# Optimization experiments

Measured on AMD Instinct MI355X. Metric: run time of the kernel, lower is better.

The kernel has to match this reference:

```python
import jax, jax.numpy as jnp
import numpy as np

N_FFT = 512
HOP = N_FFT // 4  # torch.stft default hop_length
TWO_PI = 2.0 * np.pi


def _stft_phase(x):
    """torch.stft(x, n_fft=512, return_complex=True) phase: center reflect-pad,
    rectangular window, onesided rfft. Returns [F, T'] with F = n_fft//2+1."""
    pad = N_FFT // 2
    xp = jnp.pad(x, (pad, pad), mode='reflect')
    n_frames = (xp.shape[0] - N_FFT) // HOP + 1
    idx = (np.arange(n_frames, dtype=np.int32)[:, None] * HOP
           + np.arange(N_FFT, dtype=np.int32)[None, :])
    frames = xp[idx]                      # [T', n_fft]
    spec = jnp.fft.rfft(frames, axis=-1)  # [T', F]
    return jnp.angle(spec).T              # [F, T']


def _anti_wrap(x):
    return jnp.abs(x - jnp.round(x / TWO_PI) * TWO_PI)


def _gd(p):
    # banded matmul with gd_matrix == out[f] = p[f-1] - p[f], out[0] = -p[0]
    return jnp.concatenate([-p[:1], p[:-1] - p[1:]], axis=0)


def _iaf(p):
    # banded matmul with iaf_matrix along time axis
    return jnp.concatenate([-p[:, :1], p[:, :-1] - p[:, 1:]], axis=1)


def setup_inputs() -> dict:
    key = jax.random.key(0)
    k1, k2 = jax.random.split(key)
    T = 4194304  # 2^22 samples (~262 s @ 16 kHz)
    yd = jax.random.normal(k1, (T,), dtype=jnp.float32)
    td = jax.random.normal(k2, (T,), dtype=jnp.float32)
    return {"yd": yd, "td": td}


def reference(yd, td):
    pr = _stft_phase(yd)  # [F, T']
    pg = _stft_phase(td)
    ip_loss = jnp.mean(_anti_wrap(pr - pg))
    gd_loss = jnp.mean(_anti_wrap(_gd(pr) - _gd(pg)))
    iaf_loss = jnp.mean(_anti_wrap(_iaf(pr) - _iaf(pg)))
    return (ip_loss, gd_loss, iaf_loss)
```

## Files before the change

### kernel.cpp

```cpp
#include <hip/hip_runtime.h>
#include <math.h>

#define HOP     128
#define NSLOTS  256
#define FPW     8
#define PI_F    3.14159265358979323846f
#define PI2_F   1.57079632679489661923f
#define K8      0.70710678118654752440f

struct cpx { float x, y; };
__device__ __forceinline__ cpx cadd(cpx a, cpx b){ return {a.x+b.x, a.y+b.y}; }
__device__ __forceinline__ cpx csub(cpx a, cpx b){ return {a.x-b.x, a.y-b.y}; }
__device__ __forceinline__ cpx cmul(cpx a, cpx b){
    return {fmaf(a.x,b.x,-a.y*b.y), fmaf(a.x,b.y, a.y*b.x)};
}
__device__ __forceinline__ cpx cmulc(cpx a, cpx b){
    return {fmaf(a.x,b.x, a.y*b.y), fmaf(a.y,b.x,-a.x*b.y)};
}

__device__ __forceinline__ float abs_angle(float re, float im) {
    float a = fabsf(im), b = fabsf(re);
    float mn = fminf(a, b), mx = fmaxf(a, b);
    float t = __fdividef(mn, fmaxf(mx, 1e-37f));
    float t2 = t * t;
    float p = fmaf(t2, -0.0117212f, 0.05265332f);
    p = fmaf(t2, p, -0.11643287f);
    p = fmaf(t2, p, 0.19354346f);
    p = fmaf(t2, p, -0.33262347f);
    p = fmaf(t2, p, 0.99997726f);
    float r = t * p;
    r = (a > b) ? (PI2_F - r) : r;
    r = (re < 0.f) ? (PI_F - r) : r;
    return r;
}

__device__ __forceinline__ void dft8(cpx v[8]) {
    cpx a0=cadd(v[0],v[4]), a1=cadd(v[1],v[5]), a2=cadd(v[2],v[6]), a3=cadd(v[3],v[7]);
    cpx b0=csub(v[0],v[4]), b1=csub(v[1],v[5]), b2=csub(v[2],v[6]), b3=csub(v[3],v[7]);
    b1 = cpx{K8*(b1.x+b1.y), K8*(b1.y-b1.x)};
    b2 = cpx{b2.y, -b2.x};
    b3 = cpx{K8*(b3.y-b3.x), -K8*(b3.x+b3.y)};
    cpx c0=cadd(a0,a2), c2=csub(a0,a2);
    cpx c1=cadd(a1,a3), c3=csub(a1,a3); c3 = cpx{c3.y, -c3.x};
    cpx d0=cadd(b0,b2), d2=csub(b0,b2);
    cpx d1=cadd(b1,b3), d3=csub(b1,b3); d3 = cpx{d3.y, -d3.x};
    v[0]=cadd(c0,c1); v[4]=csub(c0,c1);
    v[2]=cadd(c2,c3); v[6]=csub(c2,c3);
    v[1]=cadd(d0,d1); v[5]=csub(d0,d1);
    v[3]=cadd(d2,d3); v[7]=csub(d2,d3);
}

__global__ __launch_bounds__(256) void phase_loss_kernel(
        const float* __restrict__ y, const float* __restrict__ g,
        float* __restrict__ acc, int* __restrict__ ticket,
        float* __restrict__ out, int T, int n_frames, float inv_count) {
    __shared__ float2 xch_all[4][576];
    __shared__ float wsum[3][4];
    __shared__ int is_last;

    const int tid  = threadIdx.x;
    const int lane = tid & 63;
    const int wid  = tid >> 6;
    float2* xch = xch_all[wid];

    cpx tw1[8], tw2[8];
    #pragma unroll
    for (int k = 0; k < 8; ++k) {
        float a1 = -(2.0f * PI_F / 512.0f) * (float)(lane * k);
        __sincosf(a1, &tw1[k].y, &tw1[k].x);
        float a2 = -(2.0f * PI_F / 64.0f) * (float)((lane & 7) * k);
        __sincosf(a2, &tw2[k].y, &tw2[k].x);
    }

    float ip = 0.f, gd = 0.f, iaf = 0.f;
    cpx Cp[5];
    const int chain = blockIdx.x * 4 + wid;
    const int t0 = chain * FPW;
    const bool havep = (t0 > 0);

    auto do_frame = [&](int t, bool accum, bool hp) {
        cpx v[8];
        const int base = t * HOP - 256 + lane;
        #pragma unroll
        for (int r = 0; r < 8; ++r) {
            int j = base + r * 64;
            j = (j < 0) ? -j : j;
            j = (j >= T) ? (2 * T - 2 - j) : j;
            v[r].x = y[j]; v[r].y = g[j];
        }
        dft8(v);
        #pragma unroll
        for (int k = 1; k < 8; ++k) v[k] = cmul(v[k], tw1[k]);
        #pragma unroll
        for (int k = 0; k < 8; ++k)
            xch[k * 72 + lane] = make_float2(v[k].x, v[k].y);
        __builtin_amdgcn_s_waitcnt(0xc07f);
        __builtin_amdgcn_wave_barrier();
        {
            const int ra = (lane >> 3) * 72 + (lane & 7);
            #pragma unroll
            for (int r = 0; r < 8; ++r) {
                float2 tmp = xch[ra + r * 8];
                v[r] = cpx{tmp.x, tmp.y};
            }
        }
        dft8(v);
        #pragma unroll
        for (int k = 1; k < 8; ++k) v[k] = cmul(v[k], tw2[k]);
        #pragma unroll
        for (int k = 0; k < 8; ++k)
            xch[k * 65 + lane] = make_float2(v[k].x, v[k].y);
        __builtin_amdgcn_s_waitcnt(0xc07f);
        __builtin_amdgcn_wave_barrier();
        {
            const int ra = (lane >> 3) * 65 + (lane & 7) * 8;
            #pragma unroll
            for (int r = 0; r < 8; ++r) {
                float2 tmp = xch[ra + r];
                v[r] = cpx{tmp.x, tmp.y};
            }
        }
        dft8(v);
        cpx Cc[5];
        const int src = (64 - lane) & 63;
        #pragma unroll
        for (int jj = 0; jj < 5; ++jj) {
            cpx zk = v[jj];
            cpx zn;
            zn.x = __shfl(v[7 - jj].x, src);
            zn.y = __shfl(v[7 - jj].y, src);
            if (lane == 0) zn = v[(8 - jj) & 7];
            float ur = zk.x + zn.x, ui = zk.y - zn.y;
            float vx = zk.x - zn.x, vy = zk.y + zn.y;
            Cc[jj].x = fmaf(ur, vy, -ui * vx);
            Cc[jj].y = fmaf(ur, vx,  ui * vy);
        }
        if (accum) {
            #pragma unroll
            for (int jj = 0; jj < 4; ++jj) {
                cpx cc = Cc[jj];
                float aw = abs_angle(cc.x, cc.y);
                ip += aw;
                cpx cm;
                cm.x = __shfl_up(cc.x, 1);
                cm.y = __shfl_up(cc.y, 1);
                if (jj > 0) {
                    cpx cw;
                    cw.x = __shfl(Cc[jj - 1].x, 63);
                    cw.y = __shfl(Cc[jj - 1].y, 63);
                    if (lane == 0) cm = cw;
                }
                cpx qg = cmulc(cm, cc);
                gd += (jj == 0 && lane == 0) ? aw : abs_angle(qg.x, qg.y);
                if (hp) {
                    cpx qi = cmulc(Cp[jj], cc);
                    iaf += abs_angle(qi.x, qi.y);
                } else {
                    iaf += aw;
                }
            }
            {
                cpx cc = Cc[4];
                cpx cm;
                cm.x = __shfl(Cc[3].x, 63);
                cm.y = __shfl(Cc[3].y, 63);
                if (lane == 0) {
                    float aw = abs_angle(cc.x, cc.y);
                    ip += aw;
                    cpx qg = cmulc(cm, cc);
                    gd += abs_angle(qg.x, qg.y);
                    if (hp) {
                        cpx qi = cmulc(Cp[4], cc);
                        iaf += abs_angle(qi.x, qi.y);
                    } else {
                        iaf += aw;
                    }
                }
            }
        }
        #pragma unroll
        for (int jj = 0; jj < 5; ++jj) Cp[jj] = Cc[jj];
    };

    if (t0 < n_frames) {
        #pragma unroll 1
        for (int c = -1; c < FPW; ++c) {
            int t = t0 + c;
            if (c == -1) { if (!havep) continue; }
            else if (t >= n_frames) break;
            do_frame(t, c >= 0, havep || c > 0);
        }
    }

    __syncthreads();
    for (int off = 32; off; off >>= 1) {
        ip  += __shfl_down(ip, off);
        gd  += __shfl_down(gd, off);
        iaf += __shfl_down(iaf, off);
    }
    if (lane == 0) { wsum[0][wid] = ip; wsum[1][wid] = gd; wsum[2][wid] = iaf; }
    __syncthreads();
    if (tid == 0) {
        const int slot = (int)(blockIdx.x & (NSLOTS - 1));
        atomicAdd(acc + 0 * NSLOTS + slot, wsum[0][0] + wsum[0][1] + wsum[0][2] + wsum[0][3]);
        atomicAdd(acc + 1 * NSLOTS + slot, wsum[1][0] + wsum[1][1] + wsum[1][2] + wsum[1][3]);
        atomicAdd(acc + 2 * NSLOTS + slot, wsum[2][0] + wsum[2][1] + wsum[2][2] + wsum[2][3]);
        __threadfence();
        is_last = (atomicAdd(ticket, 1) == (int)gridDim.x - 1);
    }
    __syncthreads();
    if (is_last) {
        for (int l = 0; l < 3; l++) {
            float vv = __hip_atomic_load(acc + l * NSLOTS + tid,
                                         __ATOMIC_RELAXED, __HIP_MEMORY_SCOPE_AGENT);
            for (int off = 32; off; off >>= 1) vv += __shfl_down(vv, off);
            if (lane == 0) wsum[l][wid] = vv;
        }
        __syncthreads();
        if (tid < 3)
            out[tid] = (wsum[tid][0] + wsum[tid][1] + wsum[tid][2] + wsum[tid][3]) * inv_count;
    }
}

extern "C" void kernel_launch(void* const* d_in, const int* in_sizes, int n_in,
                              void* d_out, int out_size, void* d_ws, size_t ws_size,
                              hipStream_t stream) {
    const float* y = (const float*)d_in[0];
    const float* g = (const float*)d_in[1];
    float* out = (float*)d_out;
    float* acc = (float*)d_ws;
    int* ticket = (int*)((char*)d_ws + 3 * NSLOTS * sizeof(float));
    const int T = in_sizes[0];
    const int n_frames = T / HOP + 1;
    const int n_chains = (n_frames + FPW - 1) / FPW;
    const int n_blocks = (n_chains + 3) / 4;

    hipMemsetAsync(d_ws, 0, 3 * NSLOTS * sizeof(float) + sizeof(int), stream);
    const float inv_count = 1.0f / (257.0f * (float)n_frames);
    phase_loss_kernel<<<n_blocks, 256, 0, stream>>>(y, g, acc, ticket, out,
                                                    T, n_frames, inv_count);
}
```

Before: 138.4 us.

## Use LDS exchanges instead of shuffles, fast-path interior loads, restructure frame loop

Result: no change. 136.1 us (-1.6%).

```diff
diff --git a/kernel.cpp b/kernel.cpp
--- a/kernel.cpp
+++ b/kernel.cpp
@@ -7,6 +7,9 @@
 #define PI_F    3.14159265358979323846f
 #define PI2_F   1.57079632679489661923f
 #define K8      0.70710678118654752440f
+
+#define LDS_FENCE() do { __asm__ volatile("" ::: "memory"); \
+                         __builtin_amdgcn_wave_barrier(); } while (0)
 
 struct cpx { float x, y; };
 __device__ __forceinline__ cpx cadd(cpx a, cpx b){ return {a.x+b.x, a.y+b.y}; }
@@ -50,11 +53,12 @@
     v[3]=cadd(d2,d3); v[7]=csub(d2,d3);
 }
 
-__global__ __launch_bounds__(256) void phase_loss_kernel(
+__global__ __launch_bounds__(256, 4) void phase_loss_kernel(
         const float* __restrict__ y, const float* __restrict__ g,
         float* __restrict__ acc, int* __restrict__ ticket,
         float* __restrict__ out, int T, int n_frames, float inv_count) {
     __shared__ float2 xch_all[4][576];
+    __shared__ float2 cl_all[4][258];
     __shared__ float wsum[3][4];
     __shared__ int is_last;
 
@@ -62,6 +66,7 @@
     const int lane = tid & 63;
     const int wid  = tid >> 6;
     float2* xch = xch_all[wid];
+    float2* Cl  = cl_all[wid] + 1;
 
     cpx tw1[8], tw2[8];
     #pragma unroll
@@ -74,28 +79,34 @@
 
     float ip = 0.f, gd = 0.f, iaf = 0.f;
     cpx Cp[5];
-    const int chain = blockIdx.x * 4 + wid;
-    const int t0 = chain * FPW;
-    const bool havep = (t0 > 0);
+    const int tmax_int = (T - 256) / HOP;
 
     auto do_frame = [&](int t, bool accum, bool hp) {
         cpx v[8];
         const int base = t * HOP - 256 + lane;
-        #pragma unroll
-        for (int r = 0; r < 8; ++r) {
-            int j = base + r * 64;
-            j = (j < 0) ? -j : j;
-            j = (j >= T) ? (2 * T - 2 - j) : j;
-            v[r].x = y[j]; v[r].y = g[j];
+        if (t >= 2 && t <= tmax_int) {
+            #pragma unroll
+            for (int r = 0; r < 8; ++r) {
+                int j = base + r * 64;
+                v[r].x = y[j]; v[r].y = g[j];
+            }
+        } else {
+            #pragma unroll
+            for (int r = 0; r < 8; ++r) {
+                int j = base + r * 64;
+                j = (j < 0) ? -j : j;
+                j = (j >= T) ? (2 * T - 2 - j) : j;
+                v[r].x = y[j]; v[r].y = g[j];
+            }
         }
         dft8(v);
         #pragma unroll
         for (int k = 1; k < 8; ++k) v[k] = cmul(v[k], tw1[k]);
+        LDS_FENCE();
         #pragma unroll
         for (int k = 0; k < 8; ++k)
             xch[k * 72 + lane] = make_float2(v[k].x, v[k].y);
-        __builtin_amdgcn_s_waitcnt(0xc07f);
-        __builtin_amdgcn_wave_barrier();
+        LDS_FENCE();
         {
             const int ra = (lane >> 3) * 72 + (lane & 7);
             #pragma unroll
@@ -107,11 +118,11 @@
         dft8(v);
         #pragma unroll
         for (int k = 1; k < 8; ++k) v[k] = cmul(v[k], tw2[k]);
+        LDS_FENCE();
         #pragma unroll
         for (int k = 0; k < 8; ++k)
             xch[k * 65 + lane] = make_float2(v[k].x, v[k].y);
-        __builtin_amdgcn_s_waitcnt(0xc07f);
-        __builtin_amdgcn_wave_barrier();
+        LDS_FENCE();
         {
             const int ra = (lane >> 3) * 65 + (lane & 7) * 8;
             #pragma unroll
@@ -121,37 +132,44 @@
             }
         }
         dft8(v);
+        float2* Z = xch;
+        LDS_FENCE();
+        #pragma unroll
+        for (int j = 0; j < 8; ++j)
+            Z[lane + (j << 6)] = make_float2(v[j].x, v[j].y);
+        LDS_FENCE();
         cpx Cc[5];
-        const int src = (64 - lane) & 63;
         #pragma unroll
         for (int jj = 0; jj < 5; ++jj) {
-            cpx zk = v[jj];
-            cpx zn;
-            zn.x = __shfl(v[7 - jj].x, src);
-            zn.y = __shfl(v[7 - jj].y, src);
-            if (lane == 0) zn = v[(8 - jj) & 7];
-            float ur = zk.x + zn.x, ui = zk.y - zn.y;
-            float vx = zk.x - zn.x, vy = zk.y + zn.y;
+            const int f = lane + (jj << 6);
+            float2 tmp = Z[(512 - f) & 511];
+            float ur = v[jj].x + tmp.x, ui = v[jj].y - tmp.y;
+            float vx = v[jj].x - tmp.x, vy = v[jj].y + tmp.y;
             Cc[jj].x = fmaf(ur, vy, -ui * vx);
             Cc[jj].y = fmaf(ur, vx,  ui * vy);
         }
         if (accum) {
+            LDS_FENCE();
+            #pragma unroll
+            for (int jj = 0; jj < 4; ++jj)
+                Cl[lane + (jj << 6)] = make_float2(Cc[jj].x, Cc[jj].y);
+            if (lane == 0) Cl[256] = make_float2(Cc[4].x, Cc[4].y);
+            LDS_FENCE();
+            cpx cm[4];
+            #pragma unroll
+            for (int jj = 0; jj < 4; ++jj) {
+                float2 tmp = Cl[lane + (jj << 6) - 1];
+                cm[jj] = cpx{tmp.x, tmp.y};
+            }
+            float2 c255 = Cl[255];
             #pragma unroll
             for (int jj = 0; jj < 4; ++jj) {
                 cpx cc = Cc[jj];
                 float aw = abs_angle(cc.x, cc.y);
                 ip += aw;
-                cpx cm;
-                cm.x = __shfl_up(cc.x, 1);
-                cm.y = __shfl_up(cc.y, 1);
-                if (jj > 0) {
-                    cpx cw;
-                    cw.x = __shfl(Cc[jj - 1].x, 63);
-                    cw.y = __shfl(Cc[jj - 1].y, 63);
-                    if (lane == 0) cm = cw;
-                }
-                cpx qg = cmulc(cm, cc);
-                gd += (jj == 0 && lane == 0) ? aw : abs_angle(qg.x, qg.y);
+                cpx qg = cmulc(cm[jj], cc);
+                float gt = abs_angle(qg.x, qg.y);
+                gd += (jj == 0 && lane == 0) ? aw : gt;
                 if (hp) {
                     cpx qi = cmulc(Cp[jj], cc);
                     iaf += abs_angle(qi.x, qi.y);
@@ -159,22 +177,17 @@
                     iaf += aw;
                 }
             }
-            {
+            if (lane == 0) {
                 cpx cc = Cc[4];
-                cpx cm;
-                cm.x = __shfl(Cc[3].x, 63);
-                cm.y = __shfl(Cc[3].y, 63);
-                if (lane == 0) {
-                    float aw = abs_angle(cc.x, cc.y);
-                    ip += aw;
-                    cpx qg = cmulc(cm, cc);
-                    gd += abs_angle(qg.x, qg.y);
-                    if (hp) {
-                        cpx qi = cmulc(Cp[4], cc);
-                        iaf += abs_angle(qi.x, qi.y);
-                    } else {
-                        iaf += aw;
-                    }
+                float aw = abs_angle(cc.x, cc.y);
+                ip += aw;
+                cpx qg = cmulc(cpx{c255.x, c255.y}, cc);
+                gd += abs_angle(qg.x, qg.y);
+                if (hp) {
+                    cpx qi = cmulc(Cp[4], cc);
+                    iaf += abs_angle(qi.x, qi.y);
+                } else {
+                    iaf += aw;
                 }
             }
         }
@@ -182,15 +195,17 @@
         for (int jj = 0; jj < 5; ++jj) Cp[jj] = Cc[jj];
     };
 
-    if (t0 < n_frames) {
-        #pragma unroll 1
-        for (int c = -1; c < FPW; ++c) {
-            int t = t0 + c;
-            if (c == -1) { if (!havep) continue; }
-            else if (t >= n_frames) break;
-            do_frame(t, c >= 0, havep || c > 0);
-        }
-    }
+    const int chain   = (blockIdx.x << 2) | wid;
+    const int nchains = (int)(gridDim.x << 2);
+    const int t0 = chain * FPW;
+    int tend = t0 + FPW;
+    if (chain == nchains - 1) tend = n_frames;
+    const bool havep = (t0 > 0);
+
+    if (havep) do_frame(t0 - 1, false, false);
+    #pragma unroll 2
+    for (int t = t0; t < tend; ++t)
+        do_frame(t, true, havep || (t > t0));
 
     __syncthreads();
     for (int off = 32; off; off >>= 1) {
@@ -232,8 +247,8 @@
     int* ticket = (int*)((char*)d_ws + 3 * NSLOTS * sizeof(float));
     const int T = in_sizes[0];
     const int n_frames = T / HOP + 1;
-    const int n_chains = (n_frames + FPW - 1) / FPW;
-    const int n_blocks = (n_chains + 3) / 4;
+    int n_blocks = n_frames / (FPW * 4);
+    if (n_blocks < 1) n_blocks = 1;
 
     hipMemsetAsync(d_ws, 0, 3 * NSLOTS * sizeof(float) + sizeof(int), stream);
     const float inv_count = 1.0f / (257.0f * (float)n_frames);
```
